# Kernel optimization log

Measured on AMD Instinct MI355X. Metric: run time of the kernel, lower is better.

The kernel has to match this reference:

```python
import jax, jax.numpy as jnp
import numpy as np

B, N, C_IN, C_OUT, K, D_EMB = 32, 4096, 64, 64, 2, 16


def setup_inputs() -> dict:
    key = jax.random.key(0)
    ks = jax.random.split(key, 7)
    x = jax.random.normal(ks[0], (B, N, C_IN), jnp.float32)
    node_embeddings = jax.random.normal(ks[1], (N, D_EMB), jnp.float32)
    weights_pool = jax.random.normal(ks[2], (D_EMB, K, C_IN, C_OUT), jnp.float32) * 0.1
    bias_pool = jax.random.normal(ks[3], (D_EMB, C_OUT), jnp.float32) * 0.1
    lin_w = jax.random.normal(ks[4], (C_OUT, C_IN), jnp.float32) * 0.1
    lin_b = jax.random.normal(ks[5], (C_OUT,), jnp.float32) * 0.1
    adj = jax.random.uniform(ks[6], (N, N), jnp.float32)
    return dict(x=x, node_embeddings=node_embeddings, weights_pool=weights_pool,
                bias_pool=bias_pool, lin_w=lin_w, lin_b=lin_b, adj=adj)


def _sym_norm_adj(W):
    # W + 0.5*I, then D^{-1/2} W D^{-1/2} with D = diag(rowsum)
    n = W.shape[0]
    W = W + 0.5 * jnp.eye(n, dtype=W.dtype)
    sd = jnp.sqrt(1.0 / jnp.sum(W, axis=1))
    return sd[:, None] * W * sd[None, :]


def reference(x, node_embeddings, weights_pool, bias_pool, lin_w, lin_b, adj):
    n = node_embeddings.shape[0]
    # adaptive adjacency: softmax(relu(E E^T)) over neighbors
    supports_dyn = jax.nn.softmax(jax.nn.relu(node_embeddings @ node_embeddings.T), axis=1)
    supports = jnp.stack([jnp.eye(n, dtype=x.dtype), supports_dyn], axis=0)  # [K=2, N, N]
    # node-adaptive weights/bias generated from embeddings
    weights = jnp.einsum('nd,dkio->nkio', node_embeddings, weights_pool)  # [N,K,Cin,Cout]
    bias = node_embeddings @ bias_pool  # [N, Cout]
    # multi-hop aggregation + per-node conv
    x_g = jnp.einsum('knm,bmc->bnkc', supports, x)  # [B,N,K,Cin]
    x_gconv = jnp.einsum('bnki,nkio->bno', x_g, weights) + bias[None]  # [B,N,Cout]
    # static branch: init applies F.softmax(dim=1) to sym-normed adj, forward re-softmaxes dim=-1
    A = jax.nn.softmax(jax.nn.softmax(_sym_norm_adj(adj), axis=1), axis=-1)
    # einsum 'nm,bmc->bmc' == scale node m by sum_n A[n,m]
    scale = jnp.sum(A, axis=0)  # [N]
    x_static = (scale[None, :, None] * x) @ lin_w.T + lin_b  # [B,N,Cout]
    return x_gconv + jax.nn.sigmoid(x_static) * x_static
```

## Files before the change

### kernel.cpp

```cpp
#include <hip/hip_runtime.h>
#include <stdint.h>

#define Bdim 32
#define Ndim 4096
#define Cin  64
#define Cout 64
#define Demb 16

typedef __bf16 bf16x8 __attribute__((ext_vector_type(8)));
typedef float  f32x4  __attribute__((ext_vector_type(4)));

#define GLOBAL_AS(p) ((__attribute__((address_space(1))) void*)(p))
#define LDS_AS(p)    ((__attribute__((address_space(3))) void*)(p))
#define GLL(gp, lp)  __builtin_amdgcn_global_load_lds(GLOBAL_AS(gp), LDS_AS(lp), 16, 0, 0)

__device__ __forceinline__ uint16_t f2bf(float x) {
    union { float f; uint32_t u; } v; v.f = x;
    uint32_t r = v.u + 0x7FFFu + ((v.u >> 16) & 1u);
    return (uint16_t)(r >> 16);
}

__device__ __forceinline__ bf16x8 pack8(float4 a, float4 b) {
    union { uint16_t u[8]; bf16x8 v; } r;
    r.u[0] = f2bf(a.x); r.u[1] = f2bf(a.y); r.u[2] = f2bf(a.z); r.u[3] = f2bf(a.w);
    r.u[4] = f2bf(b.x); r.u[5] = f2bf(b.y); r.u[6] = f2bf(b.z); r.u[7] = f2bf(b.w);
    return r.v;
}

__global__ __launch_bounds__(256) void p1_prep(const float* __restrict__ E,
                                               const float* __restrict__ x,
                                               const float* __restrict__ adj,
                                               const float* __restrict__ pool,
                                               uint16_t* __restrict__ A,
                                               float* __restrict__ invA,
                                               uint16_t* __restrict__ Xtt,
                                               float* __restrict__ sd,
                                               float* __restrict__ scale,
                                               float* __restrict__ poolT) {
    __shared__ __align__(16) uint8_t smem[9232];
    const int t = threadIdx.x;
    const int blk = blockIdx.x;

    if (blk < 256) {
        float* Er_s = (float*)smem;
        float* red_s = (float*)(smem + 1024);
        const int n0 = blk * 16;
        Er_s[t] = E[n0 * Demb + t];
        __syncthreads();
        for (int half = 0; half < 2; ++half) {
            float er[8][16];
#pragma unroll
            for (int r = 0; r < 8; ++r)
#pragma unroll
                for (int d = 0; d < 16; ++d) er[r][d] = Er_s[(half * 8 + r) * 16 + d];
            float sacc[8];
#pragma unroll
            for (int r = 0; r < 8; ++r) sacc[r] = 0.f;
            for (int c = 0; c < 16; ++c) {
                const int m = c * 256 + t;
                const float4* ep = (const float4*)(E + (size_t)m * Demb);
                float4 e0 = ep[0], e1 = ep[1], e2 = ep[2], e3 = ep[3];
                float em[16] = {e0.x, e0.y, e0.z, e0.w, e1.x, e1.y, e1.z, e1.w,
                                e2.x, e2.y, e2.z, e2.w, e3.x, e3.y, e3.z, e3.w};
#pragma unroll
                for (int r = 0; r < 8; ++r) {
                    float v = 0.f;
#pragma unroll
                    for (int d = 0; d < 16; ++d) v = fmaf(er[r][d], em[d], v);
                    v = fmaxf(v, 0.f);
                    const float e = __expf(v);
                    sacc[r] += e;
                    A[(size_t)(n0 + half * 8 + r) * Ndim + m] = f2bf(e);
                }
            }
#pragma unroll
            for (int r = 0; r < 8; ++r) {
                float s = sacc[r];
#pragma unroll
                for (int off = 32; off > 0; off >>= 1) s += __shfl_down(s, off, 64);
                __syncthreads();
                if ((t & 63) == 0) red_s[t >> 6] = s;
                __syncthreads();
                if (t == 0)
                    invA[n0 + half * 8 + r] = 1.f / (red_s[0] + red_s[1] + red_s[2] + red_s[3]);
            }
            __syncthreads();
        }
    } else if (blk < 2304) {
        auto T = (uint16_t(*)[72])smem;
        const int idx = blk - 256;
        const int m0 = (idx & 63) * 64;
        const int b = idx >> 6;
        const int c = t & 63;
#pragma unroll
        for (int j = 0; j < 16; ++j) {
            const int m = (t >> 6) + j * 4;
            T[c][m] = f2bf(x[((size_t)b * Ndim + (m0 + m)) * Cin + c]);
        }
        __syncthreads();
        const int c2 = t >> 2, mo = (t & 3) * 16;
        const uint4* src = (const uint4*)&T[c2][mo];
        uint4 v0 = src[0], v1 = src[1];
        uint4* dst = (uint4*)(Xtt + (size_t)(b * Cin + c2) * Ndim + m0 + mo);
        dst[0] = v0;
        dst[1] = v1;
    } else if (blk < 6400) {
        float* red_s = (float*)smem;
        const int n = blk - 2304;
        if (n < 16) scale[n * 256 + t] = 0.f;
        const float4* ap = (const float4*)(adj + (size_t)n * Ndim);
        float s = 0.f;
#pragma unroll
        for (int q = 0; q < 4; ++q) {
            float4 a = ap[q * 256 + t];
            s += a.x + a.y + a.z + a.w;
        }
#pragma unroll
        for (int off = 32; off > 0; off >>= 1) s += __shfl_down(s, off, 64);
        if ((t & 63) == 0) red_s[t >> 6] = s;
        __syncthreads();
        if (t == 0) sd[n] = sqrtf(1.f / (red_s[0] + red_s[1] + red_s[2] + red_s[3] + 0.5f));
    } else {
        const int idx = blk - 6400;
        const int d = idx >> 2;
        const int base = (idx & 3) * 2048;
#pragma unroll
        for (int j = 0; j < 8; ++j) {
            const int e = base + j * 256 + t;
            const float v = pool[d * 8192 + e];
            poolT[d * 8192 + (e & 63) * 128 + (e >> 6)] = v;
        }
    }
}

__global__ __launch_bounds__(256) void p2_mid(const float* __restrict__ E,
                                              const float* __restrict__ adj,
                                              const float* __restrict__ sd,
                                              const float* __restrict__ poolT,
                                              const float* __restrict__ bias_pool,
                                              float* __restrict__ scale,
                                              uint16_t* __restrict__ Wt,
                                              float* __restrict__ biasn) {
    __shared__ __align__(16) uint8_t smem[16384];
    const int t = threadIdx.x;
    const int blk = blockIdx.x;

    if (blk < 256) {
        float* cs = (float*)smem;
#pragma unroll
        for (int i = 0; i < 16; ++i) cs[i * 256 + t] = 0.f;
        __syncthreads();

        const int wv = t >> 6, l = t & 63;
        const int nb = blk * 16 + wv * 4;

        float sdm[64];
#pragma unroll
        for (int i = 0; i < 16; ++i) {
            float4 s4 = *(const float4*)(sd + i * 256 + l * 4);
            sdm[i * 4 + 0] = s4.x; sdm[i * 4 + 1] = s4.y;
            sdm[i * 4 + 2] = s4.z; sdm[i * 4 + 3] = s4.w;
        }
        float colsum[64];
#pragma unroll
        for (int k = 0; k < 64; ++k) colsum[k] = 0.f;

        for (int r = 0; r < 4; ++r) {
            const int n = nb + r;
            const float sdn = sd[n];
            float e1[64];
            float s1 = 0.f;
#pragma unroll
            for (int i = 0; i < 16; ++i) {
                float4 a4 = *(const float4*)(adj + (size_t)n * Ndim + i * 256 + l * 4);
                const int c0 = i * 256 + l * 4;
                float vv[4] = {a4.x, a4.y, a4.z, a4.w};
#pragma unroll
                for (int u = 0; u < 4; ++u) {
                    const float vd = vv[u] + ((c0 + u) == n ? 0.5f : 0.f);
                    const float e = __expf(sdn * vd * sdm[i * 4 + u]);
                    e1[i * 4 + u] = e;
                    s1 += e;
                }
            }
#pragma unroll
            for (int off = 32; off > 0; off >>= 1) s1 += __shfl_xor(s1, off, 64);
            const float inv1 = 1.f / s1;
            float s2 = 0.f;
#pragma unroll
            for (int k = 0; k < 64; ++k) {
                const float e = __expf(e1[k] * inv1);
                e1[k] = e;
                s2 += e;
            }
#pragma unroll
            for (int off = 32; off > 0; off >>= 1) s2 += __shfl_xor(s2, off, 64);
            const float inv2 = 1.f / s2;
#pragma unroll
            for (int k = 0; k < 64; ++k) colsum[k] = fmaf(e1[k], inv2, colsum[k]);
        }
#pragma unroll
        for (int k = 0; k < 64; ++k)
            atomicAdd(&cs[(k >> 2) * 256 + l * 4 + (k & 3)], colsum[k]);
        __syncthreads();
#pragma unroll
        for (int i = 0; i < 16; ++i)
            atomicAdd(scale + i * 256 + t, cs[i * 256 + t]);
    } else {
        float* En = (float*)smem;
        const int idx = blk - 256;
        const int ec = idx & 7;
        const int n0 = (idx >> 3) * 32;
        En[t] = E[n0 * Demb + t];
        En[t + 256] = E[n0 * Demb + t + 256];
        __syncthreads();

        const int e0 = ec * 1024 + t * 4;
        float4 P[16];
#pragma unroll
        for (int d = 0; d < 16; ++d) P[d] = *(const float4*)(poolT + d * 8192 + e0);

        for (int g = 0; g < 32; ++g) {
            float4 acc = {0.f, 0.f, 0.f, 0.f};
#pragma unroll
            for (int d = 0; d < 16; ++d) {
                const float e = En[g * 16 + d];
                acc.x = fmaf(e, P[d].x, acc.x);
                acc.y = fmaf(e, P[d].y, acc.y);
                acc.z = fmaf(e, P[d].z, acc.z);
                acc.w = fmaf(e, P[d].w, acc.w);
            }
            union { uint16_t u[4]; uint2 v; } r;
            r.u[0] = f2bf(acc.x); r.u[1] = f2bf(acc.y);
            r.u[2] = f2bf(acc.z); r.u[3] = f2bf(acc.w);
            *(uint2*)(Wt + (size_t)(n0 + g) * 8192 + e0) = r.v;
        }

        if (ec == 0) {
            const int o = t & 63, gq = t >> 6;
#pragma unroll
            for (int gi = 0; gi < 8; ++gi) {
                const int g = gi * 4 + gq;
                float a = 0.f;
#pragma unroll
                for (int d = 0; d < 16; ++d) a = fmaf(En[g * 16 + d], bias_pool[d * 64 + o], a);
                biasn[(size_t)(n0 + g) * 64 + o] = a;
            }
        }
    }
}

#define GK 4096
#define GN 2048
#define K3_NT 64
__global__ __launch_bounds__(256) void k3_gemm(const uint16_t* __restrict__ Abf,
                                               const uint16_t* __restrict__ Bbf,
                                               const float* __restrict__ invA,
                                               uint16_t* __restrict__ Cbf) {
    __shared__ __align__(16) uint16_t As[2][128 * 64];
    __shared__ __align__(16) uint16_t Bs[2][128 * 64];
    const int t = threadIdx.x;
    const int lane = t & 63;
    const int wid = t >> 6;
    const int wr = wid >> 1;
    const int wc = wid & 1;

    const int bid = blockIdx.x;
    const int wgid = (bid & 7) * 64 + (bid >> 3);
    const int bm = (wgid >> 4) * 128;
    const int bn = (wgid & 15) * 128;

    const uint16_t* asrc[4];
    const uint16_t* bsrc[4];
    int cdst[4];
#pragma unroll
    for (int i = 0; i < 4; ++i) {
        const int c = t + i * 256;
        const int row = c >> 3, ch = c & 7;
        asrc[i] = Abf + (size_t)(bm + row) * GK + ((ch ^ (row & 7)) << 3);
        bsrc[i] = Bbf + (size_t)(bn + row) * GK + ((ch ^ (row & 7)) << 3);
        cdst[i] = c << 3;
    }

    int offA[4][2], offB[4][2];
#pragma unroll
    for (int f = 0; f < 4; ++f)
#pragma unroll
        for (int ks = 0; ks < 2; ++ks) {
            const int ra = wr * 64 + f * 16 + (lane & 15);
            offA[f][ks] = ra * 64 + (((ks * 4 + (lane >> 4)) ^ (ra & 7)) << 3);
            const int rb = wc * 64 + f * 16 + (lane & 15);
            offB[f][ks] = rb * 64 + (((ks * 4 + (lane >> 4)) ^ (rb & 7)) << 3);
        }

    f32x4 acc[4][4];
#pragma unroll
    for (int i = 0; i < 4; ++i)
#pragma unroll
        for (int j = 0; j < 4; ++j) acc[i][j] = (f32x4){0.f, 0.f, 0.f, 0.f};

#define K3_STAGE(buf, kt)                                  \
    do {                                                   \
        const size_t ko_ = (size_t)(kt) * 64;              \
        GLL(asrc[0] + ko_, &As[buf][cdst[0]]);             \
        GLL(asrc[1] + ko_, &As[buf][cdst[1]]);             \
        GLL(asrc[2] + ko_, &As[buf][cdst[2]]);             \
        GLL(asrc[3] + ko_, &As[buf][cdst[3]]);             \
        GLL(bsrc[0] + ko_, &Bs[buf][cdst[0]]);             \
        GLL(bsrc[1] + ko_, &Bs[buf][cdst[1]]);             \
        GLL(bsrc[2] + ko_, &Bs[buf][cdst[2]]);             \
        GLL(bsrc[3] + ko_, &Bs[buf][cdst[3]]);             \
    } while (0)

    K3_STAGE(0, 0);
    __syncthreads();

    for (int kt = 0; kt < K3_NT; ++kt) {
        const int cur = kt & 1;
        if (kt < K3_NT - 1) K3_STAGE(cur ^ 1, kt + 1);

        const uint16_t* Ab = As[cur];
        const uint16_t* Bb = Bs[cur];
        bf16x8 af[4][2], bfr[4][2];
#pragma unroll
        for (int ks = 0; ks < 2; ++ks) {
#pragma unroll
            for (int f = 0; f < 4; ++f) af[f][ks] = *(const bf16x8*)(Ab + offA[f][ks]);
#pragma unroll
            for (int j = 0; j < 4; ++j) bfr[j][ks] = *(const bf16x8*)(Bb + offB[j][ks]);
        }
        __builtin_amdgcn_s_setprio(1);
#pragma unroll
        for (int ks = 0; ks < 2; ++ks)
#pragma unroll
            for (int f = 0; f < 4; ++f)
#pragma unroll
                for (int j = 0; j < 4; ++j)
                    acc[f][j] = __builtin_amdgcn_mfma_f32_16x16x32_bf16(af[f][ks], bfr[j][ks], acc[f][j], 0, 0, 0);
        __builtin_amdgcn_s_setprio(0);
        __syncthreads();
    }
#undef K3_STAGE

#pragma unroll
    for (int f = 0; f < 4; ++f) {
        float invv[4];
#pragma unroll
        for (int r = 0; r < 4; ++r)
            invv[r] = invA[bm + wr * 64 + f * 16 + (lane >> 4) * 4 + r];
#pragma unroll
        for (int j = 0; j < 4; ++j)
#pragma unroll
            for (int r = 0; r < 4; ++r) {
                const int row = bm + wr * 64 + f * 16 + (lane >> 4) * 4 + r;
                const int col = bn + wc * 64 + j * 16 + (lane & 15);
                Cbf[(size_t)row * GN + col] = f2bf(acc[f][j][r] * invv[r]);
            }
    }
}

__global__ __launch_bounds__(256) void k6_gconv(const float* __restrict__ x,
                                                const uint16_t* __restrict__ XG,
                                                const uint16_t* __restrict__ Wt,
                                                const float* __restrict__ biasn,
                                                const float* __restrict__ scale,
                                                const float* __restrict__ lin_w,
                                                const float* __restrict__ lin_b,
                                                float* __restrict__ out) {
    __shared__ __align__(16) uint16_t Lws[64][72];
    const int t = threadIdx.x;
    const int n0 = blockIdx.x * 4;

    {
        const int o = t >> 2, i0 = (t & 3) * 16;
        const float4* lp = (const float4*)(lin_w + o * 64 + i0);
        float4 a0 = lp[0], a1 = lp[1], a2 = lp[2], a3 = lp[3];
        union { uint16_t u[16]; uint4 v[2]; } r;
        r.u[0] = f2bf(a0.x); r.u[1] = f2bf(a0.y); r.u[2]  = f2bf(a0.z); r.u[3]  = f2bf(a0.w);
        r.u[4] = f2bf(a1.x); r.u[5] = f2bf(a1.y); r.u[6]  = f2bf(a1.z); r.u[7]  = f2bf(a1.w);
        r.u[8] = f2bf(a2.x); r.u[9] = f2bf(a2.y); r.u[10] = f2bf(a2.z); r.u[11] = f2bf(a2.w);
        r.u[12] = f2bf(a3.x); r.u[13] = f2bf(a3.y); r.u[14] = f2bf(a3.z); r.u[15] = f2bf(a3.w);
        *(uint4*)&Lws[o][i0] = r.v[0];
        *(uint4*)&Lws[o][i0 + 8] = r.v[1];
    }

    const int w = t >> 6, lane = t & 63;
    const int n = n0 + w;
    const int l15 = lane & 15;
    const int q8 = (lane >> 4) * 8;

    bf16x8 a[2][4];
#pragma unroll
    for (int mt = 0; mt < 2; ++mt) {
        const int b = mt * 16 + l15;
        const float* xp = x + ((size_t)b * Ndim + n) * 64 + q8;
        a[mt][0] = pack8(((const float4*)xp)[0], ((const float4*)xp)[1]);
        a[mt][1] = pack8(((const float4*)(xp + 32))[0], ((const float4*)(xp + 32))[1]);
        const uint16_t* gp = XG + (size_t)n * 2048 + b * 64 + q8;
        a[mt][2] = *(const bf16x8*)gp;
        a[mt][3] = *(const bf16x8*)(gp + 32);
    }

    f32x4 accg[2][4], accs[2][4];
#pragma unroll
    for (int mt = 0; mt < 2; ++mt)
#pragma unroll
        for (int j = 0; j < 4; ++j) {
            accg[mt][j] = (f32x4){0.f, 0.f, 0.f, 0.f};
            accs[mt][j] = (f32x4){0.f, 0.f, 0.f, 0.f};
        }

    const uint16_t* wp = Wt + (size_t)n * 8192 + l15 * 128 + q8;

    __syncthreads();

#pragma unroll
    for (int ks = 0; ks < 4; ++ks) {
        bf16x8 bw[4];
#pragma unroll
        for (int j = 0; j < 4; ++j)
            bw[j] = *(const bf16x8*)(wp + j * 2048 + ks * 32);
#pragma unroll
        for (int mt = 0; mt < 2; ++mt)
#pragma unroll
            for (int j = 0; j < 4; ++j)
                accg[mt][j] = __builtin_amdgcn_mfma_f32_16x16x32_bf16(a[mt][ks], bw[j], accg[mt][j], 0, 0, 0);
        if (ks < 2) {
            bf16x8 bl[4];
#pragma unroll
            for (int j = 0; j < 4; ++j)
                bl[j] = *(const bf16x8*)&Lws[j * 16 + l15][ks * 32 + q8];
#pragma unroll
            for (int mt = 0; mt < 2; ++mt)
#pragma unroll
                for (int j = 0; j < 4; ++j)
                    accs[mt][j] = __builtin_amdgcn_mfma_f32_16x16x32_bf16(a[mt][ks], bl[j], accs[mt][j], 0, 0, 0);
        }
    }

    const float sc = scale[n];
#pragma unroll
    for (int j = 0; j < 4; ++j) {
        const int o = j * 16 + l15;
        const float bn = biasn[(size_t)n * 64 + o];
        const float lb = lin_b[o];
#pragma unroll
        for (int mt = 0; mt < 2; ++mt)
#pragma unroll
            for (int r = 0; r < 4; ++r) {
                const int b = mt * 16 + (lane >> 4) * 4 + r;
                const float gg = accg[mt][j][r] + bn;
                const float xs = sc * accs[mt][j][r] + lb;
                out[((size_t)b * Ndim + n) * 64 + o] = gg + xs / (1.f + __expf(-xs));
            }
    }
}

extern "C" void kernel_launch(void* const* d_in, const int* in_sizes, int n_in,
                              void* d_out, int out_size, void* d_ws, size_t ws_size,
                              hipStream_t stream) {
    const float* x         = (const float*)d_in[0];
    const float* E         = (const float*)d_in[1];
    const float* pool      = (const float*)d_in[2];
    const float* bias_pool = (const float*)d_in[3];
    const float* lin_w     = (const float*)d_in[4];
    const float* lin_b     = (const float*)d_in[5];
    const float* adj       = (const float*)d_in[6];
    float* out = (float*)d_out;

    uint8_t* ws = (uint8_t*)d_ws;
    uint16_t* A     = (uint16_t*)(ws);
    uint16_t* Xtt   = (uint16_t*)(ws + 33554432);
    uint16_t* XG    = (uint16_t*)(ws + 50331648);
    uint16_t* Wt    = (uint16_t*)(ws + 67108864);
    float*    biasn = (float*)   (ws + 134217728);
    float*    sd    = (float*)   (ws + 135266304);
    float*    scale = (float*)   (ws + 135282688);
    float*    poolT = (float*)   (ws + 135299072);
    float*    invA  = (float*)   (ws + 135823360);

    p1_prep<<<dim3(6464), dim3(256), 0, stream>>>(E, x, adj, pool, A, invA, Xtt, sd, scale, poolT);
    p2_mid<<<dim3(1280), dim3(256), 0, stream>>>(E, adj, sd, poolT, bias_pool, scale, Wt, biasn);
    k3_gemm<<<dim3(512), dim3(256), 0, stream>>>(A, Xtt, invA, XG);
    k6_gconv<<<dim3(1024), dim3(256), 0, stream>>>(x, XG, Wt, biasn, scale, lin_w, lin_b, out);
}
```

Baseline: 336.2 us.

## Split softmax row-sum across column chunks, halve colsum rows, prefetch gconv weights

The E·E^T exp stage in p1 now splits each 16-row block into 4 column chunks, so it runs 1024 blocks instead of 256. Each chunk writes a partial row-sum, and a new p2 branch combines the partials into invA. The adjacency colsum branch in p2 handles 2 rows per wave over 512 blocks, and the gconv kernel double-buffers its weight fragment loads so global loads overlap with MFMAs. The aim is better occupancy in the underfilled stages and hidden load latency, at the cost of an extra workspace buffer and more atomics to scale.

```diff
diff --git a/kernel.cpp b/kernel.cpp
--- a/kernel.cpp
+++ b/kernel.cpp
@@ -32,7 +32,7 @@
                                                const float* __restrict__ adj,
                                                const float* __restrict__ pool,
                                                uint16_t* __restrict__ A,
-                                               float* __restrict__ invA,
+                                               float* __restrict__ rs4,
                                                uint16_t* __restrict__ Xtt,
                                                float* __restrict__ sd,
                                                float* __restrict__ scale,
@@ -41,10 +41,12 @@
     const int t = threadIdx.x;
     const int blk = blockIdx.x;
 
-    if (blk < 256) {
+    if (blk < 1024) {
         float* Er_s = (float*)smem;
         float* red_s = (float*)(smem + 1024);
-        const int n0 = blk * 16;
+        const int n0 = (blk >> 2) * 16;
+        const int chunk = blk & 3;
+        const int m0 = chunk * 1024;
         Er_s[t] = E[n0 * Demb + t];
         __syncthreads();
         for (int half = 0; half < 2; ++half) {
@@ -56,8 +58,8 @@
             float sacc[8];
 #pragma unroll
             for (int r = 0; r < 8; ++r) sacc[r] = 0.f;
-            for (int c = 0; c < 16; ++c) {
-                const int m = c * 256 + t;
+            for (int c = 0; c < 4; ++c) {
+                const int m = m0 + c * 256 + t;
                 const float4* ep = (const float4*)(E + (size_t)m * Demb);
                 float4 e0 = ep[0], e1 = ep[1], e2 = ep[2], e3 = ep[3];
                 float em[16] = {e0.x, e0.y, e0.z, e0.w, e1.x, e1.y, e1.z, e1.w,
@@ -82,13 +84,14 @@
                 if ((t & 63) == 0) red_s[t >> 6] = s;
                 __syncthreads();
                 if (t == 0)
-                    invA[n0 + half * 8 + r] = 1.f / (red_s[0] + red_s[1] + red_s[2] + red_s[3]);
+                    rs4[(size_t)(n0 + half * 8 + r) * 4 + chunk] =
+                        red_s[0] + red_s[1] + red_s[2] + red_s[3];
             }
             __syncthreads();
         }
-    } else if (blk < 2304) {
+    } else if (blk < 3072) {
         auto T = (uint16_t(*)[72])smem;
-        const int idx = blk - 256;
+        const int idx = blk - 1024;
         const int m0 = (idx & 63) * 64;
         const int b = idx >> 6;
         const int c = t & 63;
@@ -104,9 +107,9 @@
         uint4* dst = (uint4*)(Xtt + (size_t)(b * Cin + c2) * Ndim + m0 + mo);
         dst[0] = v0;
         dst[1] = v1;
-    } else if (blk < 6400) {
+    } else if (blk < 7168) {
         float* red_s = (float*)smem;
-        const int n = blk - 2304;
+        const int n = blk - 3072;
         if (n < 16) scale[n * 256 + t] = 0.f;
         const float4* ap = (const float4*)(adj + (size_t)n * Ndim);
         float s = 0.f;
@@ -121,7 +124,7 @@
         __syncthreads();
         if (t == 0) sd[n] = sqrtf(1.f / (red_s[0] + red_s[1] + red_s[2] + red_s[3] + 0.5f));
     } else {
-        const int idx = blk - 6400;
+        const int idx = blk - 7168;
         const int d = idx >> 2;
         const int base = (idx & 3) * 2048;
 #pragma unroll
@@ -140,19 +143,21 @@
                                               const float* __restrict__ bias_pool,
                                               float* __restrict__ scale,
                                               uint16_t* __restrict__ Wt,
-                                              float* __restrict__ biasn) {
+                                              float* __restrict__ biasn,
+                                              const float* __restrict__ rs4,
+                                              float* __restrict__ invA) {
     __shared__ __align__(16) uint8_t smem[16384];
     const int t = threadIdx.x;
     const int blk = blockIdx.x;
 
-    if (blk < 256) {
+    if (blk < 512) {
         float* cs = (float*)smem;
 #pragma unroll
         for (int i = 0; i < 16; ++i) cs[i * 256 + t] = 0.f;
         __syncthreads();
 
         const int wv = t >> 6, l = t & 63;
-        const int nb = blk * 16 + wv * 4;
+        const int nb = blk * 8 + wv * 2;
 
         float sdm[64];
 #pragma unroll
@@ -165,7 +170,7 @@
 #pragma unroll
         for (int k = 0; k < 64; ++k) colsum[k] = 0.f;
 
-        for (int r = 0; r < 4; ++r) {
+        for (int r = 0; r < 2; ++r) {
             const int n = nb + r;
             const float sdn = sd[n];
             float e1[64];
@@ -206,9 +211,9 @@
 #pragma unroll
         for (int i = 0; i < 16; ++i)
             atomicAdd(scale + i * 256 + t, cs[i * 256 + t]);
-    } else {
+    } else if (blk < 1536) {
         float* En = (float*)smem;
-        const int idx = blk - 256;
+        const int idx = blk - 512;
         const int ec = idx & 7;
         const int n0 = (idx >> 3) * 32;
         En[t] = E[n0 * Demb + t];
@@ -247,6 +252,10 @@
                 biasn[(size_t)(n0 + g) * 64 + o] = a;
             }
         }
+    } else {
+        const int n = (blk - 1536) * 256 + t;
+        const float4 v = *(const float4*)(rs4 + (size_t)n * 4);
+        invA[n] = 1.f / (v.x + v.y + v.z + v.w);
     }
 }
 
@@ -412,31 +421,58 @@
 
     const uint16_t* wp = Wt + (size_t)n * 8192 + l15 * 128 + q8;
 
+    bf16x8 bw0[4], bw1[4];
+#pragma unroll
+    for (int j = 0; j < 4; ++j) bw0[j] = *(const bf16x8*)(wp + j * 2048);
+
     __syncthreads();
 
 #pragma unroll
-    for (int ks = 0; ks < 4; ++ks) {
-        bf16x8 bw[4];
+    for (int j = 0; j < 4; ++j) bw1[j] = *(const bf16x8*)(wp + j * 2048 + 32);
+#pragma unroll
+    for (int mt = 0; mt < 2; ++mt)
 #pragma unroll
         for (int j = 0; j < 4; ++j)
-            bw[j] = *(const bf16x8*)(wp + j * 2048 + ks * 32);
+            accg[mt][j] = __builtin_amdgcn_mfma_f32_16x16x32_bf16(a[mt][0], bw0[j], accg[mt][j], 0, 0, 0);
+    {
+        bf16x8 bl[4];
+#pragma unroll
+        for (int j = 0; j < 4; ++j) bl[j] = *(const bf16x8*)&Lws[j * 16 + l15][q8];
 #pragma unroll
         for (int mt = 0; mt < 2; ++mt)
 #pragma unroll
             for (int j = 0; j < 4; ++j)
-                accg[mt][j] = __builtin_amdgcn_mfma_f32_16x16x32_bf16(a[mt][ks], bw[j], accg[mt][j], 0, 0, 0);
-        if (ks < 2) {
-            bf16x8 bl[4];
+                accs[mt][j] = __builtin_amdgcn_mfma_f32_16x16x32_bf16(a[mt][0], bl[j], accs[mt][j], 0, 0, 0);
+    }
+#pragma unroll
+    for (int j = 0; j < 4; ++j) bw0[j] = *(const bf16x8*)(wp + j * 2048 + 64);
+#pragma unroll
+    for (int mt = 0; mt < 2; ++mt)
+#pragma unroll
+        for (int j = 0; j < 4; ++j)
+            accg[mt][j] = __builtin_amdgcn_mfma_f32_16x16x32_bf16(a[mt][1], bw1[j], accg[mt][j], 0, 0, 0);
+    {
+        bf16x8 bl[4];
+#pragma unroll
+        for (int j = 0; j < 4; ++j) bl[j] = *(const bf16x8*)&Lws[j * 16 + l15][32 + q8];
+#pragma unroll
+        for (int mt = 0; mt < 2; ++mt)
 #pragma unroll
             for (int j = 0; j < 4; ++j)
-                bl[j] = *(const bf16x8*)&Lws[j * 16 + l15][ks * 32 + q8];
-#pragma unroll
-            for (int mt = 0; mt < 2; ++mt)
-#pragma unroll
-                for (int j = 0; j < 4; ++j)
-                    accs[mt][j] = __builtin_amdgcn_mfma_f32_16x16x32_bf16(a[mt][ks], bl[j], accs[mt][j], 0, 0, 0);
-        }
-    }
+                accs[mt][j] = __builtin_amdgcn_mfma_f32_16x16x32_bf16(a[mt][1], bl[j], accs[mt][j], 0, 0, 0);
+    }
+#pragma unroll
+    for (int j = 0; j < 4; ++j) bw1[j] = *(const bf16x8*)(wp + j * 2048 + 96);
+#pragma unroll
+    for (int mt = 0; mt < 2; ++mt)
+#pragma unroll
+        for (int j = 0; j < 4; ++j)
+            accg[mt][j] = __builtin_amdgcn_mfma_f32_16x16x32_bf16(a[mt][2], bw0[j], accg[mt][j], 0, 0, 0);
+#pragma unroll
+    for (int mt = 0; mt < 2; ++mt)
+#pragma unroll
+        for (int j = 0; j < 4; ++j)
+            accg[mt][j] = __builtin_amdgcn_mfma_f32_16x16x32_bf16(a[mt][3], bw1[j], accg[mt][j], 0, 0, 0);
 
     const float sc = scale[n];
 #pragma unroll
@@ -478,9 +514,10 @@
     float*    scale = (float*)   (ws + 135282688);
     float*    poolT = (float*)   (ws + 135299072);
     float*    invA  = (float*)   (ws + 135823360);
-
-    p1_prep<<<dim3(6464), dim3(256), 0, stream>>>(E, x, adj, pool, A, invA, Xtt, sd, scale, poolT);
-    p2_mid<<<dim3(1280), dim3(256), 0, stream>>>(E, adj, sd, poolT, bias_pool, scale, Wt, biasn);
+    float*    rs4   = (float*)   (ws + 135839744);
+
+    p1_prep<<<dim3(7232), dim3(256), 0, stream>>>(E, x, adj, pool, A, rs4, Xtt, sd, scale, poolT);
+    p2_mid<<<dim3(1552), dim3(256), 0, stream>>>(E, adj, sd, poolT, bias_pool, scale, Wt, biasn, rs4, invA);
     k3_gemm<<<dim3(512), dim3(256), 0, stream>>>(A, Xtt, invA, XG);
     k6_gconv<<<dim3(1024), dim3(256), 0, stream>>>(x, XG, Wt, biasn, scale, lin_w, lin_b, out);
 }
```

New measurement: 369.2 us. 1.1x slower.
